# Performance work log

Measured on AMD Instinct MI355X. Metric: run time of the kernel, lower is better.

Reference implementation:

```python
import jax, jax.numpy as jnp
import numpy as np

B, T, C = 2, 2048, 2048
H, DK, DV, K = 16, 128, 128, 4
KEY_DIM = H * DK
VALUE_DIM = H * DV
CONV_DIM = 2 * KEY_DIM + VALUE_DIM
EPS = 1e-6


def setup_inputs() -> dict:
    key = jax.random.key(0)
    ks = jax.random.split(key, 6)
    s = 0.02
    return {
        "x": jax.random.normal(ks[0], (B, T, C), jnp.float32),
        "input_pos": jnp.arange(T, dtype=jnp.int32),
        "W_qkvz": jax.random.normal(ks[1], (C, CONV_DIM + VALUE_DIM), jnp.float32) * s,
        "W_b": jax.random.normal(ks[2], (C, H), jnp.float32) * s,
        "W_a": jax.random.normal(ks[3], (C, H), jnp.float32) * s,
        "conv_w": jax.random.normal(ks[4], (CONV_DIM, 1, K), jnp.float32) * 0.3,
        "norm_w": jnp.ones((DV,), jnp.float32),
        "W_out": jax.random.normal(ks[5], (VALUE_DIM, C), jnp.float32) * s,
        "conv_state": jnp.zeros((B, CONV_DIM, K), jnp.float32),
        "recurrent_state": jnp.zeros((B, H, DK, DV), jnp.float32),
    }


def _l2norm(a):
    return a / jnp.maximum(jnp.linalg.norm(a, axis=-1, keepdims=True), 1e-12)


def reference(x, input_pos, W_qkvz, W_b, W_a, conv_w, norm_w, W_out,
              conv_state, recurrent_state):
    Bx, Tx, Cx = x.shape
    # reset state when sequence starts at position 0
    keep = 1.0 - (input_pos[0] == 0).astype(x.dtype)
    conv_state = conv_state * keep
    recurrent_state = recurrent_state * keep

    qkvz = x @ W_qkvz                                  # [B,T,conv_dim+value_dim]
    qkv, z = qkvz[..., :CONV_DIM], qkvz[..., CONV_DIM:]
    z = z.reshape(Bx, Tx, H, DV)
    beta = jax.nn.sigmoid(x @ W_b)                     # [B,T,H]
    alpha = jax.nn.sigmoid(x @ W_a)                    # [B,T,H]

    # depthwise causal conv with carried conv_state prefix
    conv_in = jnp.concatenate([conv_state, qkv.transpose(0, 2, 1)], axis=-1)  # [B,conv_dim,K+T]
    y = jax.lax.conv_general_dilated(
        conv_in, conv_w, window_strides=(1,), padding='VALID',
        dimension_numbers=('NCH', 'OIH', 'NCH'), feature_group_count=CONV_DIM)
    y = jax.nn.silu(y[:, :, -Tx:]).transpose(0, 2, 1)  # [B,T,conv_dim]

    q, k, v = jnp.split(y, [KEY_DIM, 2 * KEY_DIM], axis=-1)
    q = _l2norm(q.reshape(Bx, Tx, H, DK))
    k = _l2norm(k.reshape(Bx, Tx, H, DK))
    v = v.reshape(Bx, Tx, H, DV)

    def step(state, xs):
        q_i, k_i, v_i, a_i, b_i = xs                    # [B,H,Dk],[B,H,Dk],[B,H,Dv],[B,H],[B,H]
        new_state = (a_i[..., None, None] * state
                     + b_i[..., None, None] * (k_i[..., :, None] * v_i[..., None, :]))
        out_i = jnp.einsum('bhk,bhkv->bhv', q_i, new_state)
        return new_state, out_i

    xs = (q.transpose(1, 0, 2, 3), k.transpose(1, 0, 2, 3), v.transpose(1, 0, 2, 3),
          alpha.transpose(1, 0, 2), beta.transpose(1, 0, 2))
    _, outs = jax.lax.scan(step, recurrent_state, xs)   # outs: [T,B,H,Dv]
    output = outs.transpose(1, 0, 2, 3)                 # [B,T,H,Dv]

    # RMSNorm over head_v_dim, then gate by sigmoid(z)
    output = output * jax.lax.rsqrt(jnp.mean(output * output, axis=-1, keepdims=True) + EPS) * norm_w
    output = output * jax.nn.sigmoid(z)
    return output.reshape(Bx, Tx, -1) @ W_out
```

## Files before the change

### kernel.cpp

```cpp
#include <hip/hip_runtime.h>
#include <hip/hip_bf16.h>
#include <math.h>

#define Bb 2
#define Tt 2048
#define Cc 2048
#define Hh 16
#define CONVD 6144
#define Mrows 4096
#define NCHUNK 32

typedef __attribute__((ext_vector_type(8))) short short8v;
typedef __attribute__((ext_vector_type(4))) float floatx4;

__device__ __forceinline__ unsigned short f2bf(float f) {
    __hip_bfloat16 h = __float2bfloat16(f);
    return __builtin_bit_cast(unsigned short, h);
}

__device__ __forceinline__ void load_lds16(const void* g, void* l) {
    __builtin_amdgcn_global_load_lds(
        (const __attribute__((address_space(1))) void*)g,
        (__attribute__((address_space(3))) void*)l, 16, 0, 0);
}

__device__ __forceinline__ int swz8(int col) {
    return col ^ (((col >> 5) & 3) << 3);
}

#define LGKM0 asm volatile("s_waitcnt lgkmcnt(0)" ::: "memory")
#define VMC4  asm volatile("s_waitcnt vmcnt(4)" ::: "memory")
#define VMC0  asm volatile("s_waitcnt vmcnt(0)" ::: "memory")
#define SCHB  __builtin_amdgcn_sched_barrier(0)
#define SBAR  __builtin_amdgcn_s_barrier()

__global__ __launch_bounds__(256) void transpose_cast2(
    const float* __restrict__ W1, unsigned short* __restrict__ WT1,
    const float* __restrict__ W2, unsigned short* __restrict__ WT2)
{
    const float* W; unsigned short* WT; int Nn;
    if (blockIdx.z == 0) { W = W1; WT = WT1; Nn = 8192; }
    else                 { W = W2; WT = WT2; Nn = 2048; if (blockIdx.x >= 64) return; }
    __shared__ float tile[32][33];
    const int n0 = blockIdx.x * 32;
    const int k0 = blockIdx.y * 32;
    const int tx = threadIdx.x & 31;
    const int ty = threadIdx.x >> 5;
#pragma unroll
    for (int r = ty; r < 32; r += 8)
        tile[r][tx] = W[(size_t)(k0 + r) * Nn + n0 + tx];
    __syncthreads();
#pragma unroll
    for (int r = ty; r < 32; r += 8)
        WT[(size_t)(n0 + r) * 2048 + k0 + tx] = f2bf(tile[tx][r]);
}

__global__ __launch_bounds__(512) void gemm256(
    const unsigned short* __restrict__ A, const unsigned short* __restrict__ Bt,
    float* __restrict__ C1, float* __restrict__ C2,
    int Kk, int lda, int ldb)
{
    __shared__ __align__(16) unsigned short A_lds[2][256 * 32];
    __shared__ __align__(16) unsigned short B_lds[2][256 * 32];

    const int tid  = threadIdx.x;
    const int wid  = tid >> 6;
    const int lane = tid & 63;
    const int wr = wid >> 2, wc = wid & 3;
    const int l15 = lane & 15, kq = lane >> 4;
    const int rdsw = (kq ^ ((l15 >> 1) & 3)) * 8;
    const int rr = lane >> 2;
    const int ch = (lane & 3) ^ ((lane >> 3) & 3);

    const int bid = blockIdx.y * 32 + blockIdx.x;
    const int xcd = bid & 7;
    const int idx = bid >> 3;
    const int block_m = ((xcd >> 2) * 8 + (idx >> 3)) * 256;
    const int block_n = ((xcd & 3) * 8 + (idx & 7)) * 256;

    const int NT = Kk >> 5;

#define STAGE256(t) do {                                                     \
    const int kk0 = (t) << 5;                                                \
    unsigned short* la = &A_lds[(t) & 1][0];                                 \
    unsigned short* lb = &B_lds[(t) & 1][0];                                 \
    _Pragma("unroll")                                                        \
    for (int i_ = 0; i_ < 2; ++i_) {                                         \
        const int g_ = wid * 2 + i_;                                         \
        load_lds16(A + (size_t)(block_m + g_ * 16 + rr) * lda + kk0 + ch * 8,\
                   la + g_ * 512);                                           \
        load_lds16(Bt + (size_t)(block_n + g_ * 16 + rr) * ldb + kk0 + ch * 8,\
                   lb + g_ * 512);                                           \
    }                                                                        \
} while (0)

    floatx4 acc[8][4] = {};

    STAGE256(0);
    STAGE256(1);
    VMC4; SCHB; SBAR; SCHB;

    for (int t = 0; t < NT; ++t) {
        const unsigned short* la = &A_lds[t & 1][0];
        const unsigned short* lb = &B_lds[t & 1][0];
        short8v af[8], bf[4];
#pragma unroll
        for (int mf = 0; mf < 8; ++mf)
            af[mf] = *(const short8v*)(la + (wr * 128 + mf * 16 + l15) * 32 + rdsw);
#pragma unroll
        for (int nf = 0; nf < 4; ++nf)
            bf[nf] = *(const short8v*)(lb + (wc * 64 + nf * 16 + l15) * 32 + rdsw);
        LGKM0; SCHB;
        SBAR;
        SCHB;
        if (t + 2 < NT) STAGE256(t + 2);
        SCHB;
        __builtin_amdgcn_s_setprio(1);
#pragma unroll
        for (int mf = 0; mf < 8; ++mf)
#pragma unroll
            for (int nf = 0; nf < 4; ++nf)
                acc[mf][nf] = __builtin_amdgcn_mfma_f32_16x16x32_bf16(
                    af[mf], bf[nf], acc[mf][nf], 0, 0, 0);
        __builtin_amdgcn_s_setprio(0);
        SCHB;
        if (t + 2 < NT)      { VMC4; }
        else if (t + 1 < NT) { VMC0; }
        SCHB; SBAR; SCHB;
    }

    float* Cp; int col0; size_t ldc;
    if (block_n < 6144) { Cp = C1; col0 = block_n;        ldc = 6144; }
    else                { Cp = C2; col0 = block_n - 6144; ldc = 2048; }
#pragma unroll
    for (int mf = 0; mf < 8; ++mf)
#pragma unroll
        for (int nf = 0; nf < 4; ++nf)
#pragma unroll
            for (int r = 0; r < 4; ++r) {
                int row = block_m + wr * 128 + mf * 16 + kq * 4 + r;
                int col = col0 + wc * 64 + nf * 16 + l15;
                Cp[(size_t)row * ldc + col] = acc[mf][nf][r];
            }
#undef STAGE256
}

__global__ __launch_bounds__(256) void gemm_bf16(
    const unsigned short* __restrict__ A, const unsigned short* __restrict__ Bt,
    float* __restrict__ C, int Kk, int lda, int ldb, int ldc)
{
    __shared__ __align__(16) unsigned short A_lds[128 * 64];
    __shared__ __align__(16) unsigned short B_lds[128 * 64];

    const int tid = threadIdx.x;
    const int wv = tid >> 6;
    const int lane = tid & 63;
    const int wr = wv >> 1, wc = wv & 1;
    const int l15 = lane & 15, kq = lane >> 4;
    const int rsw = (l15 & 7) << 3;

    const int nwg = gridDim.x * gridDim.y;
    const int bid = blockIdx.y * gridDim.x + blockIdx.x;
    const int wgid = (bid & 7) * (nwg >> 3) + (bid >> 3);
    const int block_m = (wgid / gridDim.x) * 128;
    const int block_n = (wgid % gridDim.x) * 128;

    const int srow = lane >> 3;
    const int scol = ((lane & 7) ^ srow) << 3;

    floatx4 acc[4][4] = {};

    for (int k0 = 0; k0 < Kk; k0 += 64) {
#pragma unroll
        for (int i = 0; i < 4; ++i) {
            const int lq = wv * 4 + i;
            const unsigned short* asrc =
                A + (size_t)(block_m + lq * 8 + srow) * lda + k0 + scol;
            load_lds16(asrc, &A_lds[lq * 512]);
            const unsigned short* bsrc =
                Bt + (size_t)(block_n + lq * 8 + srow) * ldb + k0 + scol;
            load_lds16(bsrc, &B_lds[lq * 512]);
        }
        __syncthreads();

#pragma unroll
        for (int kk = 0; kk < 2; ++kk) {
            short8v af[4], bf[4];
#pragma unroll
            for (int mf = 0; mf < 4; ++mf) {
                const int row = wr * 64 + mf * 16 + l15;
                af[mf] = *(const short8v*)&A_lds[row * 64 + ((kk * 32 + kq * 8) ^ rsw)];
            }
#pragma unroll
            for (int nf = 0; nf < 4; ++nf) {
                const int row = wc * 64 + nf * 16 + l15;
                bf[nf] = *(const short8v*)&B_lds[row * 64 + ((kk * 32 + kq * 8) ^ rsw)];
            }
#pragma unroll
            for (int mf = 0; mf < 4; ++mf)
#pragma unroll
                for (int nf = 0; nf < 4; ++nf)
                    acc[mf][nf] = __builtin_amdgcn_mfma_f32_16x16x32_bf16(
                        af[mf], bf[nf], acc[mf][nf], 0, 0, 0);
        }
        __syncthreads();
    }

#pragma unroll
    for (int mf = 0; mf < 4; ++mf)
#pragma unroll
        for (int nf = 0; nf < 4; ++nf)
#pragma unroll
            for (int r = 0; r < 4; ++r) {
                int row = block_m + wr * 64 + mf * 16 + kq * 4 + r;
                int col = block_n + wc * 64 + nf * 16 + l15;
                C[(size_t)row * ldc + col] = acc[mf][nf][r];
            }
}

__global__ __launch_bounds__(256) void ab_kernel(
    const float* __restrict__ x, const float* __restrict__ W_b,
    const float* __restrict__ W_a, float* __restrict__ beta,
    float* __restrict__ alpha, unsigned short* __restrict__ xb)
{
    const int row = blockIdx.x;
    const int tid = threadIdx.x;
    float acc[32];
#pragma unroll
    for (int u = 0; u < 32; ++u) acc[u] = 0.f;

    for (int k = tid; k < Cc; k += 256) {
        float xv = x[(size_t)row * Cc + k];
        xb[(size_t)row * Cc + k] = f2bf(xv);
        const float4* wb = (const float4*)(W_b + (size_t)k * 16);
        const float4* wa = (const float4*)(W_a + (size_t)k * 16);
#pragma unroll
        for (int u = 0; u < 4; ++u) {
            float4 b4 = wb[u];
            float4 a4 = wa[u];
            acc[u * 4 + 0] = fmaf(xv, b4.x, acc[u * 4 + 0]);
            acc[u * 4 + 1] = fmaf(xv, b4.y, acc[u * 4 + 1]);
            acc[u * 4 + 2] = fmaf(xv, b4.z, acc[u * 4 + 2]);
            acc[u * 4 + 3] = fmaf(xv, b4.w, acc[u * 4 + 3]);
            acc[16 + u * 4 + 0] = fmaf(xv, a4.x, acc[16 + u * 4 + 0]);
            acc[16 + u * 4 + 1] = fmaf(xv, a4.y, acc[16 + u * 4 + 1]);
            acc[16 + u * 4 + 2] = fmaf(xv, a4.z, acc[16 + u * 4 + 2]);
            acc[16 + u * 4 + 3] = fmaf(xv, a4.w, acc[16 + u * 4 + 3]);
        }
    }
#pragma unroll
    for (int u = 0; u < 32; ++u) {
        float v = acc[u];
        for (int off = 32; off > 0; off >>= 1) v += __shfl_down(v, off);
        acc[u] = v;
    }
    __shared__ float red[4][32];
    const int wv = tid >> 6;
    if ((tid & 63) == 0) {
#pragma unroll
        for (int u = 0; u < 32; ++u) red[wv][u] = acc[u];
    }
    __syncthreads();
    if (tid < 32) {
        float v = red[0][tid] + red[1][tid] + red[2][tid] + red[3][tid];
        float s = 1.f / (1.f + expf(-v));
        if (tid < 16) beta[(size_t)row * 16 + tid] = s;
        else          alpha[(size_t)row * 16 + (tid - 16)] = s;
    }
}

__global__ __launch_bounds__(128) void conv_kernel(
    const float* __restrict__ qkv, const float* __restrict__ conv_w,
    const float* __restrict__ conv_state, const int* __restrict__ input_pos,
    float* __restrict__ qn, float* __restrict__ kn, float* __restrict__ vv)
{
    const int tc = blockIdx.x;
    const int hs = blockIdx.y;
    const int b  = blockIdx.z;
    const int lane = threadIdx.x;
    const int kind = hs >> 4;
    const int h = hs & 15;
    const int c = kind * 2048 + h * 128 + lane;
    const int t0 = tc * 16;
    const float keep = (input_pos[0] == 0) ? 0.f : 1.f;

    const float4 w4 = *(const float4*)(conv_w + (size_t)c * 4);

    float win0, win1, win2;
    {
        float tmp[3];
#pragma unroll
        for (int j = 0; j < 3; ++j) {
            int tau = t0 - 3 + j;
            tmp[j] = (tau >= 0) ? qkv[(size_t)(b * Tt + tau) * CONVD + c]
                   : keep * conv_state[((size_t)b * CONVD + c) * 4 + (tau + 4)];
        }
        win0 = tmp[0]; win1 = tmp[1]; win2 = tmp[2];
    }

    float y[16];
    __shared__ float red[16][2];
#pragma unroll
    for (int i = 0; i < 16; ++i) {
        float xv = qkv[(size_t)(b * Tt + t0 + i) * CONVD + c];
        float a = fmaf(w4.x, win0, fmaf(w4.y, win1, fmaf(w4.z, win2, w4.w * xv)));
        float yy = a / (1.f + expf(-a));
        win0 = win1; win1 = win2; win2 = xv;
        if (kind == 2) {
            vv[(size_t)(b * Tt + t0 + i) * 2048 + h * 128 + lane] = yy;
        } else {
            float sq = yy * yy;
            for (int off = 32; off > 0; off >>= 1) sq += __shfl_down(sq, off);
            if ((lane & 63) == 0) red[i][lane >> 6] = sq;
            y[i] = yy;
        }
    }
    if (kind == 2) return;
    __syncthreads();
#pragma unroll
    for (int i = 0; i < 16; ++i) {
        float tot = red[i][0] + red[i][1];
        float inv = 1.f / fmaxf(sqrtf(tot), 1e-12f);
        float outv = y[i] * inv;
        const size_t oidx = (size_t)(b * Tt + t0 + i) * 2048 + h * 128 + lane;
        if (kind == 0) qn[oidx] = outv;
        else           kn[oidx] = outv;
    }
}

__global__ __launch_bounds__(256) void chunk_prep(
    const float* __restrict__ kn, const float* __restrict__ vv,
    const float* __restrict__ alpha, const float* __restrict__ beta,
    float* __restrict__ logc_g, float* __restrict__ Mbuf)
{
    const int c = blockIdx.x, h = blockIdx.y, b = blockIdx.z;
    const int tid = threadIdx.x;
    const size_t bh = (size_t)b * Hh + h;

    __shared__ float K_lds[32][128];
    __shared__ float V_lds[32][128];
    __shared__ float logc_lds[64];
    __shared__ float b_lds[64];
    __shared__ float wk_lds[64];

    if (tid < 64) {
        const int row = b * Tt + c * 64 + tid;
        float a = alpha[(size_t)row * 16 + h];
        float la = logf(a);
#pragma unroll
        for (int d = 1; d < 64; d <<= 1) {
            float n = __shfl_up(la, d);
            if (tid >= d) la += n;
        }
        logc_lds[tid] = la;
        logc_g[bh * Tt + c * 64 + tid] = la;
        b_lds[tid] = beta[(size_t)row * 16 + h];
    }
    __syncthreads();
    if (tid < 64) {
        wk_lds[tid] = expf(logc_lds[63] - logc_lds[tid]) * b_lds[tid];
    }
    __syncthreads();

    const int ti = tid >> 4;
    const int tj = tid & 15;
    const int tj8sw = swz8(tj * 8);
    float acc[8][8];
#pragma unroll
    for (int i = 0; i < 8; ++i)
#pragma unroll
        for (int j = 0; j < 8; ++j) acc[i][j] = 0.f;

    for (int half = 0; half < 2; ++half) {
        {
            const int sl = tid >> 3;
            const int c0 = (tid & 7) * 16;
            const int grow = b * Tt + c * 64 + half * 32 + sl;
            const float4* kp = (const float4*)(kn + (size_t)grow * 2048 + h * 128 + c0);
            const float4* vp = (const float4*)(vv + (size_t)grow * 2048 + h * 128 + c0);
#pragma unroll
            for (int u = 0; u < 4; ++u) {
                const int cl = c0 + u * 4;
                *(float4*)(&K_lds[sl][cl]) = kp[u];
                *(float4*)(&V_lds[sl][swz8(cl)]) = vp[u];
            }
        }
        __syncthreads();
#pragma unroll 4
        for (int s = 0; s < 32; ++s) {
            float w = wk_lds[half * 32 + s];
            float4 k0 = *(const float4*)(&K_lds[s][ti * 8]);
            float4 k1 = *(const float4*)(&K_lds[s][ti * 8 + 4]);
            float4 v0 = *(const float4*)(&V_lds[s][tj8sw]);
            float4 v1 = *(const float4*)(&V_lds[s][tj8sw + 4]);
            float wk[8] = {w*k0.x, w*k0.y, w*k0.z, w*k0.w, w*k1.x, w*k1.y, w*k1.z, w*k1.w};
            float vf[8] = {v0.x, v0.y, v0.z, v0.w, v1.x, v1.y, v1.z, v1.w};
#pragma unroll
            for (int i = 0; i < 8; ++i)
#pragma unroll
                for (int j = 0; j < 8; ++j)
                    acc[i][j] = fmaf(wk[i], vf[j], acc[i][j]);
        }
        __syncthreads();
    }
    float* mb = Mbuf + ((bh * NCHUNK) + c) * 16384;
#pragma unroll
    for (int i = 0; i < 8; ++i) {
        float4 o0 = {acc[i][0], acc[i][1], acc[i][2], acc[i][3]};
        float4 o1 = {acc[i][4], acc[i][5], acc[i][6], acc[i][7]};
        *(float4*)(mb + (size_t)(ti * 8 + i) * 128 + tj * 8) = o0;
        *(float4*)(mb + (size_t)(ti * 8 + i) * 128 + tj * 8 + 4) = o1;
    }
}

__global__ __launch_bounds__(256) void state_scan(
    float* __restrict__ Mbuf, const float* __restrict__ logc_g,
    const float* __restrict__ rec_state, const int* __restrict__ input_pos)
{
    const size_t g = (size_t)blockIdx.x * 256 + threadIdx.x;
    const int bh = (int)(g >> 14);
    const float keep = (input_pos[0] == 0) ? 0.f : 1.f;

    float S = keep * rec_state[g];
    const float* lc = logc_g + (size_t)bh * Tt;
    float* base = Mbuf + (size_t)(g & ~16383ull) * NCHUNK + (g & 16383);
#pragma unroll 4
    for (int c = 0; c < NCHUNK; ++c) {
        float Atot = expf(lc[c * 64 + 63]);
        float m = base[(size_t)c * 16384];
        base[(size_t)c * 16384] = S;
        S = fmaf(Atot, S, m);
    }
}

__global__ __launch_bounds__(256) void chunk_out(
    const float* __restrict__ qn, const float* __restrict__ kn,
    const float* __restrict__ vv, const float* __restrict__ beta,
    const float* __restrict__ logc_g, const float* __restrict__ Sstates,
    const float* __restrict__ norm_w, const float* __restrict__ zbuf,
    unsigned short* __restrict__ gated_b)
{
    const int c = blockIdx.x, h = blockIdx.y, b = blockIdx.z;
    const int tid = threadIdx.x;
    const int ti = tid >> 4;
    const int tj = tid & 15;
    const size_t bh = (size_t)b * Hh + h;
    const int row0 = b * Tt + c * 64;

    __shared__ float Q_lds[64][132];
    __shared__ float Bf[64 * 68];
    __shared__ float At[64][68];
    __shared__ float logc_s[64], b_s[64];

    {
        const int r = tid >> 2, c0 = (tid & 3) * 32;
        const float4* qp = (const float4*)(qn + (size_t)(row0 + r) * 2048 + h * 128 + c0);
#pragma unroll
        for (int u = 0; u < 8; ++u)
            *(float4*)(&Q_lds[r][c0 + u * 4]) = qp[u];
    }
    if (tid < 64) {
        logc_s[tid] = logc_g[bh * Tt + c * 64 + tid];
        b_s[tid] = beta[(size_t)(row0 + tid) * 16 + h];
    }

    float acc_a[4][4] = {};
    for (int kh = 0; kh < 2; ++kh) {
        __syncthreads();
        {
            const int s = tid >> 2, c0 = (tid & 3) * 16;
            const float* kp = kn + (size_t)(row0 + s) * 2048 + h * 128 + kh * 64 + c0;
#pragma unroll
            for (int u = 0; u < 16; ++u)
                Bf[(c0 + u) * 68 + s] = kp[u];
        }
        __syncthreads();
#pragma unroll 4
        for (int kk = 0; kk < 64; ++kk) {
            float a[4];
#pragma unroll
            for (int r = 0; r < 4; ++r) a[r] = Q_lds[ti * 4 + r][kh * 64 + kk];
            float4 bq = *(const float4*)(&Bf[kk * 68 + tj * 4]);
            float bb[4] = {bq.x, bq.y, bq.z, bq.w};
#pragma unroll
            for (int r = 0; r < 4; ++r)
#pragma unroll
                for (int cc = 0; cc < 4; ++cc)
                    acc_a[r][cc] = fmaf(a[r], bb[cc], acc_a[r][cc]);
        }
    }

#pragma unroll
    for (int r = 0; r < 4; ++r) {
        const int t = ti * 4 + r;
        const float lct = logc_s[t];
#pragma unroll
        for (int cc = 0; cc < 4; ++cc) {
            const int s = tj * 4 + cc;
            float w = (s <= t) ? expf(lct - logc_s[s]) * b_s[s] : 0.f;
            At[t][s] = w * acc_a[r][cc];
        }
    }

    float o[4][8] = {};
    const float* Sbase = Sstates + (bh * NCHUNK + c) * 16384;
    const int tj8sw = swz8(tj * 8);
    for (int kb = 0; kb < 8; ++kb) {
        __syncthreads();
        {
            const int rr = tid >> 4;
            const int cl = (tid & 15) * 8;
            const int sw = swz8(cl);
            const float4* sp = (const float4*)(Sbase + (size_t)(kb * 16 + rr) * 128 + cl);
            *(float4*)(&Bf[rr * 132 + sw]) = sp[0];
            *(float4*)(&Bf[rr * 132 + sw + 4]) = sp[1];
        }
        __syncthreads();
#pragma unroll
        for (int kk = 0; kk < 16; ++kk) {
            float a[4];
#pragma unroll
            for (int r = 0; r < 4; ++r) a[r] = Q_lds[ti * 4 + r][kb * 16 + kk];
            float4 s0 = *(const float4*)(&Bf[kk * 132 + tj8sw]);
            float4 s1 = *(const float4*)(&Bf[kk * 132 + tj8sw + 4]);
            float sv[8] = {s0.x, s0.y, s0.z, s0.w, s1.x, s1.y, s1.z, s1.w};
#pragma unroll
            for (int r = 0; r < 4; ++r)
#pragma unroll
                for (int j = 0; j < 8; ++j)
                    o[r][j] = fmaf(a[r], sv[j], o[r][j]);
        }
    }
#pragma unroll
    for (int r = 0; r < 4; ++r) {
        const float ct = expf(logc_s[ti * 4 + r]);
#pragma unroll
        for (int j = 0; j < 8; ++j) o[r][j] *= ct;
    }

    for (int sh = 0; sh < 2; ++sh) {
        __syncthreads();
        {
            const int rr = tid >> 3;
            const int c0 = (tid & 7) * 16;
            const float4* vp = (const float4*)(vv + (size_t)(row0 + sh * 32 + rr) * 2048 + h * 128 + c0);
#pragma unroll
            for (int u = 0; u < 4; ++u) {
                const int cl = c0 + u * 4;
                *(float4*)(&Bf[rr * 132 + swz8(cl)]) = vp[u];
            }
        }
        __syncthreads();
#pragma unroll 2
        for (int sp = 0; sp < 32; ++sp) {
            const int s = sh * 32 + sp;
            float a[4];
#pragma unroll
            for (int r = 0; r < 4; ++r) a[r] = At[ti * 4 + r][s];
            float4 v0 = *(const float4*)(&Bf[sp * 132 + tj8sw]);
            float4 v1 = *(const float4*)(&Bf[sp * 132 + tj8sw + 4]);
            float vf[8] = {v0.x, v0.y, v0.z, v0.w, v1.x, v1.y, v1.z, v1.w};
#pragma unroll
            for (int r = 0; r < 4; ++r)
#pragma unroll
                for (int j = 0; j < 8; ++j)
                    o[r][j] = fmaf(a[r], vf[j], o[r][j]);
        }
    }

#pragma unroll
    for (int r = 0; r < 4; ++r) {
        float ss = 0.f;
#pragma unroll
        for (int j = 0; j < 8; ++j) ss = fmaf(o[r][j], o[r][j], ss);
        ss += __shfl_xor(ss, 1);
        ss += __shfl_xor(ss, 2);
        ss += __shfl_xor(ss, 4);
        ss += __shfl_xor(ss, 8);
        const float scale = rsqrtf(ss * (1.f / 128.f) + 1e-6f);
        const int t = ti * 4 + r;
        const float* zp = zbuf + (size_t)(row0 + t) * 2048 + h * 128 + tj * 8;
        unsigned short* gp = gated_b + (size_t)(row0 + t) * 2048 + h * 128 + tj * 8;
#pragma unroll
        for (int j = 0; j < 8; ++j) {
            float zv = zp[j];
            float g = o[r][j] * scale * norm_w[tj * 8 + j] * (1.f / (1.f + expf(-zv)));
            gp[j] = f2bf(g);
        }
    }
}

extern "C" void kernel_launch(void* const* d_in, const int* in_sizes, int n_in,
                              void* d_out, int out_size, void* d_ws, size_t ws_size,
                              hipStream_t stream) {
    (void)in_sizes; (void)n_in; (void)out_size; (void)ws_size;
    const float* x          = (const float*)d_in[0];
    const int*   input_pos  = (const int*)d_in[1];
    const float* W_qkvz     = (const float*)d_in[2];
    const float* W_b        = (const float*)d_in[3];
    const float* W_a        = (const float*)d_in[4];
    const float* conv_w     = (const float*)d_in[5];
    const float* norm_w     = (const float*)d_in[6];
    const float* W_out      = (const float*)d_in[7];
    const float* conv_state = (const float*)d_in[8];
    const float* rec_state  = (const float*)d_in[9];
    float* out = (float*)d_out;
    float* ws  = (float*)d_ws;

    float* qkv   = ws;
    float* Mbuf  = ws;
    unsigned short* gated_b = (unsigned short*)(ws + 16777216);
    float* qn    = ws + 25165824ull;
    float* kn    = qn + 8388608ull;
    float* vv    = kn + 8388608ull;
    unsigned short* xb  = (unsigned short*)qn;
    unsigned short* WqT = (unsigned short*)(qn + 4194304ull);
    float* zbuf  = vv + 8388608ull;
    unsigned short* WoT = (unsigned short*)(zbuf + 8388608ull);
    float* alpha = zbuf + 8388608ull + 2097152ull;
    float* beta  = alpha + 65536ull;
    float* logc  = beta + 65536ull;

    transpose_cast2<<<dim3(256, 64, 2), 256, 0, stream>>>(W_qkvz, WqT, W_out, WoT);
    ab_kernel<<<Mrows, 256, 0, stream>>>(x, W_b, W_a, beta, alpha, xb);

    gemm256<<<dim3(8192 / 256, Mrows / 256), 512, 0, stream>>>(
        xb, WqT, qkv, zbuf, 2048, 2048, 2048);
    conv_kernel<<<dim3(Tt / 16, 48, Bb), 128, 0, stream>>>(
        qkv, conv_w, conv_state, input_pos, qn, kn, vv);
    chunk_prep<<<dim3(NCHUNK, Hh, Bb), 256, 0, stream>>>(
        kn, vv, alpha, beta, logc, Mbuf);
    state_scan<<<2048, 256, 0, stream>>>(Mbuf, logc, rec_state, input_pos);
    chunk_out<<<dim3(NCHUNK, Hh, Bb), 256, 0, stream>>>(
        qn, kn, vv, beta, logc, Mbuf, norm_w, zbuf, gated_b);
    gemm_bf16<<<dim3(2048 / 128, Mrows / 128), 256, 0, stream>>>(
        gated_b, WoT, out, 2048, 2048, 2048, 2048);
}
```

Before: 534.8 us.

## Restructure gemm256 into BK=64 four-phase pipeline with interleaved staging

The main projection GEMM now uses a K tile of 64 instead of 32. Each K step is split into four phases over M halves and K subtiles, and the global-to-LDS loads for the next tile are spread across those phases so they overlap with MFMA work. LDS is laid out as rows of 64 with an XOR swizzle. This halves the number of K iterations and barriers per byte loaded, but doubles LDS use to 128KB, adds more barriers inside each step, and replaces the deeper two-ahead prefetch with a one-ahead double buffer.

Result: no change. 533.0 us (-0.3%).

```diff
diff --git a/kernel.cpp b/kernel.cpp
--- a/kernel.cpp
+++ b/kernel.cpp
@@ -29,7 +29,6 @@
 }
 
 #define LGKM0 asm volatile("s_waitcnt lgkmcnt(0)" ::: "memory")
-#define VMC4  asm volatile("s_waitcnt vmcnt(4)" ::: "memory")
 #define VMC0  asm volatile("s_waitcnt vmcnt(0)" ::: "memory")
 #define SCHB  __builtin_amdgcn_sched_barrier(0)
 #define SBAR  __builtin_amdgcn_s_barrier()
@@ -55,22 +54,36 @@
         WT[(size_t)(n0 + r) * 2048 + k0 + tx] = f2bf(tile[tx][r]);
 }
 
+__device__ __forceinline__ void stage_ht(
+    const unsigned short* __restrict__ G, unsigned short* lds_buf,
+    int ld, int k0, int h, int wid, int lane)
+{
+#pragma unroll
+    for (int j = 0; j < 2; ++j) {
+        const int base_row = h * 128 + j * 64 + wid * 8;
+        const int row = base_row + (lane >> 3);
+        const int ch = (lane & 7) ^ (lane >> 3);
+        load_lds16(G + (size_t)row * ld + k0 + ch * 8, lds_buf + base_row * 64);
+    }
+}
+
+__device__ __forceinline__ short8v frag(const unsigned short* lds_buf, int R, int g) {
+    return *(const short8v*)(lds_buf + R * 64 + ((g ^ (R & 7)) << 3));
+}
+
 __global__ __launch_bounds__(512) void gemm256(
     const unsigned short* __restrict__ A, const unsigned short* __restrict__ Bt,
     float* __restrict__ C1, float* __restrict__ C2,
     int Kk, int lda, int ldb)
 {
-    __shared__ __align__(16) unsigned short A_lds[2][256 * 32];
-    __shared__ __align__(16) unsigned short B_lds[2][256 * 32];
+    __shared__ __align__(16) unsigned short A_lds[2][256 * 64];
+    __shared__ __align__(16) unsigned short B_lds[2][256 * 64];
 
     const int tid  = threadIdx.x;
     const int wid  = tid >> 6;
     const int lane = tid & 63;
     const int wr = wid >> 2, wc = wid & 3;
     const int l15 = lane & 15, kq = lane >> 4;
-    const int rdsw = (kq ^ ((l15 >> 1) & 3)) * 8;
-    const int rr = lane >> 2;
-    const int ch = (lane & 3) ^ ((lane >> 3) & 3);
 
     const int bid = blockIdx.y * 32 + blockIdx.x;
     const int xcd = bid & 7;
@@ -78,56 +91,63 @@
     const int block_m = ((xcd >> 2) * 8 + (idx >> 3)) * 256;
     const int block_n = ((xcd & 3) * 8 + (idx & 7)) * 256;
 
-    const int NT = Kk >> 5;
-
-#define STAGE256(t) do {                                                     \
-    const int kk0 = (t) << 5;                                                \
-    unsigned short* la = &A_lds[(t) & 1][0];                                 \
-    unsigned short* lb = &B_lds[(t) & 1][0];                                 \
-    _Pragma("unroll")                                                        \
-    for (int i_ = 0; i_ < 2; ++i_) {                                         \
-        const int g_ = wid * 2 + i_;                                         \
-        load_lds16(A + (size_t)(block_m + g_ * 16 + rr) * lda + kk0 + ch * 8,\
-                   la + g_ * 512);                                           \
-        load_lds16(Bt + (size_t)(block_n + g_ * 16 + rr) * ldb + kk0 + ch * 8,\
-                   lb + g_ * 512);                                           \
-    }                                                                        \
+    const unsigned short* Ag = A + (size_t)block_m * lda;
+    const unsigned short* Bg = Bt + (size_t)block_n * ldb;
+
+    const int NT = Kk >> 6;
+
+    floatx4 acc[8][4] = {};
+
+    stage_ht(Ag, &A_lds[0][0], lda, 0, 0, wid, lane);
+    stage_ht(Ag, &A_lds[0][0], lda, 0, 1, wid, lane);
+    stage_ht(Bg, &B_lds[0][0], ldb, 0, 0, wid, lane);
+    stage_ht(Bg, &B_lds[0][0], ldb, 0, 1, wid, lane);
+    VMC0; SCHB; SBAR;
+
+#define PHASE(mh, ks, STAGECODE, VMCODE) do {                                 \
+    short8v af[4], bf[4];                                                     \
+    _Pragma("unroll")                                                         \
+    for (int m4 = 0; m4 < 4; ++m4)                                            \
+        af[m4] = frag(la, wr * 128 + ((mh) * 4 + m4) * 16 + l15, (ks) * 4 + kq); \
+    _Pragma("unroll")                                                         \
+    for (int nf = 0; nf < 4; ++nf)                                            \
+        bf[nf] = frag(lb, wc * 64 + nf * 16 + l15, (ks) * 4 + kq);            \
+    STAGECODE;                                                                \
+    SBAR;                                                                     \
+    LGKM0; SCHB;                                                              \
+    __builtin_amdgcn_s_setprio(1);                                            \
+    _Pragma("unroll")                                                         \
+    for (int m4 = 0; m4 < 4; ++m4)                                            \
+        _Pragma("unroll")                                                     \
+        for (int nf = 0; nf < 4; ++nf)                                        \
+            acc[(mh) * 4 + m4][nf] = __builtin_amdgcn_mfma_f32_16x16x32_bf16( \
+                af[m4], bf[nf], acc[(mh) * 4 + m4][nf], 0, 0, 0);             \
+    __builtin_amdgcn_s_setprio(0);                                            \
+    SCHB;                                                                     \
+    VMCODE;                                                                   \
+    SBAR;                                                                     \
 } while (0)
-
-    floatx4 acc[8][4] = {};
-
-    STAGE256(0);
-    STAGE256(1);
-    VMC4; SCHB; SBAR; SCHB;
 
     for (int t = 0; t < NT; ++t) {
         const unsigned short* la = &A_lds[t & 1][0];
         const unsigned short* lb = &B_lds[t & 1][0];
-        short8v af[8], bf[4];
-#pragma unroll
-        for (int mf = 0; mf < 8; ++mf)
-            af[mf] = *(const short8v*)(la + (wr * 128 + mf * 16 + l15) * 32 + rdsw);
-#pragma unroll
-        for (int nf = 0; nf < 4; ++nf)
-            bf[nf] = *(const short8v*)(lb + (wc * 64 + nf * 16 + l15) * 32 + rdsw);
-        LGKM0; SCHB;
-        SBAR;
-        SCHB;
-        if (t + 2 < NT) STAGE256(t + 2);
-        SCHB;
-        __builtin_amdgcn_s_setprio(1);
-#pragma unroll
-        for (int mf = 0; mf < 8; ++mf)
-#pragma unroll
-            for (int nf = 0; nf < 4; ++nf)
-                acc[mf][nf] = __builtin_amdgcn_mfma_f32_16x16x32_bf16(
-                    af[mf], bf[nf], acc[mf][nf], 0, 0, 0);
-        __builtin_amdgcn_s_setprio(0);
-        SCHB;
-        if (t + 2 < NT)      { VMC4; }
-        else if (t + 1 < NT) { VMC0; }
-        SCHB; SBAR; SCHB;
-    }
+        unsigned short* sa = &A_lds[(t + 1) & 1][0];
+        unsigned short* sb = &B_lds[(t + 1) & 1][0];
+        const int k0n = (t + 1) << 6;
+        const bool more = (t + 1 < NT);
+
+        PHASE(0, 0,
+              { if (more) { stage_ht(Ag, sa, lda, k0n, 0, wid, lane);
+                            stage_ht(Ag, sa, lda, k0n, 1, wid, lane); } },
+              {});
+        PHASE(1, 0,
+              { if (more) { stage_ht(Bg, sb, ldb, k0n, 0, wid, lane);
+                            stage_ht(Bg, sb, ldb, k0n, 1, wid, lane); } },
+              {});
+        PHASE(0, 1, {}, {});
+        PHASE(1, 1, {}, { if (more) { VMC0; SCHB; } });
+    }
+#undef PHASE
 
     float* Cp; int col0; size_t ldc;
     if (block_n < 6144) { Cp = C1; col0 = block_n;        ldc = 6144; }
@@ -142,7 +162,6 @@
                 int col = col0 + wc * 64 + nf * 16 + l15;
                 Cp[(size_t)row * ldc + col] = acc[mf][nf][r];
             }
-#undef STAGE256
 }
 
 __global__ __launch_bounds__(256) void gemm_bf16(
```

## Deepen GEMM LDS pipeline to four stages and double-buffer state tiles

Applied to the files above, without the earlier changes.

The 256x256 bf16 GEMM moves from a 2-deep to a 4-deep LDS ring buffer, prefetching three k-tiles ahead. This removes one barrier per iteration and relaxes the vmcnt waits. The chunked output kernel now double-buffers the recurrent-state tiles through registers, so the global load of the next 16-row block overlaps the FMA loop on the current one. The GEMM LDS footprint doubles to 128 KB, which may limit occupancy. The chunk kernel's Bf buffer must also be large enough for two 16x132 slices.

Result: faster. 517.9 us (-3.2%).

```diff
diff --git a/kernel.cpp b/kernel.cpp
--- a/kernel.cpp
+++ b/kernel.cpp
@@ -29,6 +29,7 @@
 }
 
 #define LGKM0 asm volatile("s_waitcnt lgkmcnt(0)" ::: "memory")
+#define VMC8  asm volatile("s_waitcnt vmcnt(8)" ::: "memory")
 #define VMC4  asm volatile("s_waitcnt vmcnt(4)" ::: "memory")
 #define VMC0  asm volatile("s_waitcnt vmcnt(0)" ::: "memory")
 #define SCHB  __builtin_amdgcn_sched_barrier(0)
@@ -60,17 +61,18 @@
     float* __restrict__ C1, float* __restrict__ C2,
     int Kk, int lda, int ldb)
 {
-    __shared__ __align__(16) unsigned short A_lds[2][256 * 32];
-    __shared__ __align__(16) unsigned short B_lds[2][256 * 32];
+    __shared__ __align__(16) unsigned short A_lds[4][256 * 32];
+    __shared__ __align__(16) unsigned short B_lds[4][256 * 32];
 
     const int tid  = threadIdx.x;
     const int wid  = tid >> 6;
     const int lane = tid & 63;
     const int wr = wid >> 2, wc = wid & 3;
     const int l15 = lane & 15, kq = lane >> 4;
-    const int rdsw = (kq ^ ((l15 >> 1) & 3)) * 8;
+
     const int rr = lane >> 2;
-    const int ch = (lane & 3) ^ ((lane >> 3) & 3);
+    const int cs = (lane & 3) ^ ((rr >> 1) & 3);
+    const int fch = (kq ^ ((l15 >> 1) & 3)) << 3;
 
     const int bid = blockIdx.y * 32 + blockIdx.x;
     const int xcd = bid & 7;
@@ -78,43 +80,46 @@
     const int block_m = ((xcd >> 2) * 8 + (idx >> 3)) * 256;
     const int block_n = ((xcd & 3) * 8 + (idx & 7)) * 256;
 
+    const unsigned short* Ag = A + (size_t)block_m * lda;
+    const unsigned short* Bg = Bt + (size_t)block_n * ldb;
+
     const int NT = Kk >> 5;
 
-#define STAGE256(t) do {                                                     \
-    const int kk0 = (t) << 5;                                                \
-    unsigned short* la = &A_lds[(t) & 1][0];                                 \
-    unsigned short* lb = &B_lds[(t) & 1][0];                                 \
+#define STG(bi, kk0) do {                                                    \
+    unsigned short* la_ = &A_lds[(bi)][0];                                   \
+    unsigned short* lb_ = &B_lds[(bi)][0];                                   \
     _Pragma("unroll")                                                        \
-    for (int i_ = 0; i_ < 2; ++i_) {                                         \
-        const int g_ = wid * 2 + i_;                                         \
-        load_lds16(A + (size_t)(block_m + g_ * 16 + rr) * lda + kk0 + ch * 8,\
-                   la + g_ * 512);                                           \
-        load_lds16(Bt + (size_t)(block_n + g_ * 16 + rr) * ldb + kk0 + ch * 8,\
-                   lb + g_ * 512);                                           \
+    for (int j_ = 0; j_ < 2; ++j_) {                                         \
+        const int brow = wid * 32 + j_ * 16;                                 \
+        load_lds16(Ag + (size_t)(brow + rr) * lda + (kk0) + cs * 8,          \
+                   la_ + brow * 32);                                         \
+        load_lds16(Bg + (size_t)(brow + rr) * ldb + (kk0) + cs * 8,          \
+                   lb_ + brow * 32);                                         \
     }                                                                        \
 } while (0)
 
     floatx4 acc[8][4] = {};
 
-    STAGE256(0);
-    STAGE256(1);
-    VMC4; SCHB; SBAR; SCHB;
+    STG(0, 0);
+    STG(1, 32);
+    STG(2, 64);
+    VMC8; SCHB; SBAR;
 
     for (int t = 0; t < NT; ++t) {
-        const unsigned short* la = &A_lds[t & 1][0];
-        const unsigned short* lb = &B_lds[t & 1][0];
+        const unsigned short* la = &A_lds[t & 3][0];
+        const unsigned short* lb = &B_lds[t & 3][0];
+
         short8v af[8], bf[4];
 #pragma unroll
         for (int mf = 0; mf < 8; ++mf)
-            af[mf] = *(const short8v*)(la + (wr * 128 + mf * 16 + l15) * 32 + rdsw);
+            af[mf] = *(const short8v*)(la + (wr * 128 + mf * 16 + l15) * 32 + fch);
 #pragma unroll
         for (int nf = 0; nf < 4; ++nf)
-            bf[nf] = *(const short8v*)(lb + (wc * 64 + nf * 16 + l15) * 32 + rdsw);
+            bf[nf] = *(const short8v*)(lb + (wc * 64 + nf * 16 + l15) * 32 + fch);
+
+        if (t + 3 < NT) STG((t + 3) & 3, (t + 3) << 5);
+
         LGKM0; SCHB;
-        SBAR;
-        SCHB;
-        if (t + 2 < NT) STAGE256(t + 2);
-        SCHB;
         __builtin_amdgcn_s_setprio(1);
 #pragma unroll
         for (int mf = 0; mf < 8; ++mf)
@@ -124,10 +129,14 @@
                     af[mf], bf[nf], acc[mf][nf], 0, 0, 0);
         __builtin_amdgcn_s_setprio(0);
         SCHB;
-        if (t + 2 < NT)      { VMC4; }
-        else if (t + 1 < NT) { VMC0; }
-        SCHB; SBAR; SCHB;
-    }
+        if (t + 1 < NT) {
+            if      (t + 3 < NT) { VMC8; }
+            else if (t + 2 < NT) { VMC4; }
+            else                 { VMC0; }
+            SCHB; SBAR;
+        }
+    }
+#undef STG
 
     float* Cp; int col0; size_t ldc;
     if (block_n < 6144) { Cp = C1; col0 = block_n;        ldc = 6144; }
@@ -142,7 +151,6 @@
                 int col = col0 + wc * 64 + nf * 16 + l15;
                 Cp[(size_t)row * ldc + col] = acc[mf][nf][r];
             }
-#undef STAGE256
 }
 
 __global__ __launch_bounds__(256) void gemm_bf16(
@@ -505,24 +513,33 @@
     float o[4][8] = {};
     const float* Sbase = Sstates + (bh * NCHUNK + c) * 16384;
     const int tj8sw = swz8(tj * 8);
+    const int rws = tid >> 4;
+    const int cl = (tid & 15) * 8;
+    const int sw = swz8(cl);
+    float* Sb0 = Bf;
+    float* Sb1 = Bf + 2112;
+    {
+        __syncthreads();
+        const float4* sp = (const float4*)(Sbase + (size_t)rws * 128 + cl);
+        *(float4*)(&Sb0[rws * 132 + sw]) = sp[0];
+        *(float4*)(&Sb0[rws * 132 + sw + 4]) = sp[1];
+        __syncthreads();
+    }
     for (int kb = 0; kb < 8; ++kb) {
-        __syncthreads();
-        {
-            const int rr = tid >> 4;
-            const int cl = (tid & 15) * 8;
-            const int sw = swz8(cl);
-            const float4* sp = (const float4*)(Sbase + (size_t)(kb * 16 + rr) * 128 + cl);
-            *(float4*)(&Bf[rr * 132 + sw]) = sp[0];
-            *(float4*)(&Bf[rr * 132 + sw + 4]) = sp[1];
-        }
-        __syncthreads();
+        const float* src = (kb & 1) ? Sb1 : Sb0;
+        float* dst = (kb & 1) ? Sb0 : Sb1;
+        float4 nv0, nv1;
+        if (kb < 7) {
+            const float4* sp = (const float4*)(Sbase + (size_t)((kb + 1) * 16 + rws) * 128 + cl);
+            nv0 = sp[0]; nv1 = sp[1];
+        }
 #pragma unroll
         for (int kk = 0; kk < 16; ++kk) {
             float a[4];
 #pragma unroll
             for (int r = 0; r < 4; ++r) a[r] = Q_lds[ti * 4 + r][kb * 16 + kk];
-            float4 s0 = *(const float4*)(&Bf[kk * 132 + tj8sw]);
-            float4 s1 = *(const float4*)(&Bf[kk * 132 + tj8sw + 4]);
+            float4 s0 = *(const float4*)(&src[kk * 132 + tj8sw]);
+            float4 s1 = *(const float4*)(&src[kk * 132 + tj8sw + 4]);
             float sv[8] = {s0.x, s0.y, s0.z, s0.w, s1.x, s1.y, s1.z, s1.w};
 #pragma unroll
             for (int r = 0; r < 4; ++r)
@@ -530,6 +547,11 @@
                 for (int j = 0; j < 8; ++j)
                     o[r][j] = fmaf(a[r], sv[j], o[r][j]);
         }
+        if (kb < 7) {
+            *(float4*)(&dst[rws * 132 + sw]) = nv0;
+            *(float4*)(&dst[rws * 132 + sw + 4]) = nv1;
+        }
+        __syncthreads();
     }
 #pragma unroll
     for (int r = 0; r < 4; ++r) {
@@ -546,8 +568,8 @@
             const float4* vp = (const float4*)(vv + (size_t)(row0 + sh * 32 + rr) * 2048 + h * 128 + c0);
 #pragma unroll
             for (int u = 0; u < 4; ++u) {
-                const int cl = c0 + u * 4;
-                *(float4*)(&Bf[rr * 132 + swz8(cl)]) = vp[u];
+                const int clv = c0 + u * 4;
+                *(float4*)(&Bf[rr * 132 + swz8(clv)]) = vp[u];
             }
         }
         __syncthreads();
```
